# Kernel optimization log

Measured on AMD Instinct MI355X. Metric: run time of the kernel, lower is better.

The kernel has to match this reference:

```python
import jax, jax.numpy as jnp
import numpy as np

B, H, W, C = 4, 64, 64, 512
R = max(1, C // 8)  # reduced = channels // 8

def setup_inputs() -> dict:
    key = jax.random.key(0)
    ks = jax.random.split(key, 5)
    x  = jax.random.normal(ks[0], (B, H, W, C), dtype=jnp.float32)
    Wq = jax.random.normal(ks[1], (C, R), dtype=jnp.float32) * (1.0 / np.sqrt(C))
    Wk = jax.random.normal(ks[2], (C, R), dtype=jnp.float32) * (1.0 / np.sqrt(C))
    Wv = jax.random.normal(ks[3], (C, C), dtype=jnp.float32) * (1.0 / np.sqrt(C))
    Wo = jax.random.normal(ks[4], (C, C), dtype=jnp.float32) * (1.0 / np.sqrt(C))
    gamma = jnp.float32(1.0)
    return {"x": x, "Wq": Wq, "Wk": Wk, "Wv": Wv, "Wo": Wo, "gamma": gamma}

def reference(x, Wq, Wk, Wv, Wo, gamma):
    b, h, w, c = x.shape
    hw = h * w
    r = Wq.shape[1]
    xf = x.reshape(b, hw, c)                      # [B, HW, C]; 1x1 conv == channel matmul
    q = xf @ Wq                                   # [B, HW, R]
    k = xf @ Wk                                   # [B, HW, R]
    v = xf @ Wv                                   # [B, HW, C]
    scale = jnp.sqrt(jnp.asarray(r, dtype=x.dtype))
    scores = jnp.einsum('bnr,bmr->bnm', q, k) / scale   # [B, HW, HW]
    attn = jax.nn.softmax(scores, axis=-1)
    attended = jnp.einsum('bnm,bmc->bnc', attn, v)      # [B, HW, C]
    out = attended @ Wo                                  # out_conv (1x1, no bias)
    return (gamma * out.reshape(b, h, w, c) + x)
```

## Files before the change

kernel.cpp:

```cpp
#include <hip/hip_runtime.h>

typedef unsigned short u16;
typedef short short8 __attribute__((ext_vector_type(8)));
typedef float f32x4 __attribute__((ext_vector_type(4)));

#define LOG2E 1.44269504088896340736f

__device__ __forceinline__ u16 f2bf(float f) {
  unsigned u = __builtin_bit_cast(unsigned, f);
  u += 0x7fffu + ((u >> 16) & 1u);
  return (u16)(u >> 16);
}

__device__ __forceinline__ unsigned cvt_pk_bf16(float lo, float hi) {
  unsigned r;
  asm("v_cvt_pk_bf16_f32 %0, %1, %2" : "=v"(r) : "v"(lo), "v"(hi));
  return r;
}

__global__ __launch_bounds__(256) void k_convert_x(const float* __restrict__ x,
                                                   u16* __restrict__ xb) {
  int i = blockIdx.x * 256 + threadIdx.x;
  float4 v = ((const float4*)x)[i];
  ushort4 o;
  o.x = f2bf(v.x); o.y = f2bf(v.y); o.z = f2bf(v.z); o.w = f2bf(v.w);
  ((ushort4*)xb)[i] = o;
}

__global__ __launch_bounds__(256) void k_wcat(const float* __restrict__ Wq,
                                              const float* __restrict__ Wk,
                                              const float* __restrict__ Wv,
                                              const float* __restrict__ Wo,
                                              u16* __restrict__ wcatT) {
  __shared__ float wo8T[8 * 512];
  int bid = blockIdx.x, t = threadIdx.x;
  if (bid < 8) {
    for (int i = t; i < 8192; i += 256) {
      int j = bid * 16 + (i >> 9);
      int c = i & 511;
      float v = (j < 64) ? Wq[c * 64 + j] * (0.125f * LOG2E) : Wk[c * 64 + (j - 64)];
      wcatT[j * 512 + c] = f2bf(v);
    }
  } else {
    int j0 = (bid - 8) * 8;
    for (int i = t; i < 4096; i += 256) {
      int jj = i >> 9, kk = i & 511;
      wo8T[jj * 512 + kk] = Wo[kk * 512 + j0 + jj];
    }
    __syncthreads();
    for (int c = t; c < 512; c += 256) {
      const float4* wr = (const float4*)(Wv + c * 512);
      float acc[8] = {};
      for (int kk = 0; kk < 128; kk++) {
        float4 v = wr[kk];
#pragma unroll
        for (int jj = 0; jj < 8; jj++) {
          float4 wa = *(const float4*)&wo8T[jj * 512 + kk * 4];
          acc[jj] += v.x * wa.x + v.y * wa.y + v.z * wa.z + v.w * wa.w;
        }
      }
#pragma unroll
      for (int jj = 0; jj < 8; jj++)
        wcatT[(128 + j0 + jj) * 512 + c] = f2bf(acc[jj]);
    }
  }
}

__global__ __launch_bounds__(256) void k_qkv(const u16* __restrict__ xb,
                                             const u16* __restrict__ wcatT,
                                             u16* __restrict__ q,
                                             u16* __restrict__ kf,
                                             u16* __restrict__ vf) {
  __shared__ u16 lds[16384];
  int tid = threadIdx.x;
  int w = tid >> 6, lane = tid & 63;
  int fr = lane & 15, fg = lane >> 4;
  int wm = w >> 1, wn = w & 1;
  int rowbase = blockIdx.y * 128;
  int jbase = blockIdx.x * 128;
  f32x4 acc[4][4] = {};

  for (int kb = 0; kb < 512; kb += 64) {
    __syncthreads();
#pragma unroll
    for (int n = 0; n < 4; n++) {
      int lin = n * 4096 + tid * 16;
      int row = lin >> 7;
      int src = (((lin >> 4) & 7) * 16) ^ ((row & 7) << 4);
      const char* ga = (const char*)(xb + (size_t)(rowbase + row) * 512 + kb) + src;
      __builtin_amdgcn_global_load_lds(
          (const __attribute__((address_space(1))) void*)ga,
          (__attribute__((address_space(3))) void*)((char*)lds + n * 4096 + (w << 10)),
          16, 0, 0);
    }
#pragma unroll
    for (int n = 0; n < 4; n++) {
      int lin = n * 4096 + tid * 16;
      int row = lin >> 7;
      int src = (((lin >> 4) & 7) * 16) ^ ((row & 7) << 4);
      const char* ga = (const char*)(wcatT + (size_t)(jbase + row) * 512 + kb) + src;
      __builtin_amdgcn_global_load_lds(
          (const __attribute__((address_space(1))) void*)ga,
          (__attribute__((address_space(3))) void*)((char*)lds + 16384 + n * 4096 + (w << 10)),
          16, 0, 0);
    }
    __syncthreads();
    short8 af[4][2], bfr[4][2];
#pragma unroll
    for (int mt = 0; mt < 4; mt++)
#pragma unroll
      for (int ks = 0; ks < 2; ks++) {
        int row = wm * 64 + mt * 16 + fr;
        int off = row * 128 + ((ks * 64 + fg * 16) ^ ((row & 7) << 4));
        af[mt][ks] = *(const short8*)((const char*)lds + off);
      }
#pragma unroll
    for (int nt = 0; nt < 4; nt++)
#pragma unroll
      for (int ks = 0; ks < 2; ks++) {
        int j = wn * 64 + nt * 16 + fr;
        int off = 16384 + j * 128 + ((ks * 64 + fg * 16) ^ ((j & 7) << 4));
        bfr[nt][ks] = *(const short8*)((const char*)lds + off);
      }
#pragma unroll
    for (int ks = 0; ks < 2; ks++)
#pragma unroll
      for (int mt = 0; mt < 4; mt++)
#pragma unroll
        for (int nt = 0; nt < 4; nt++)
          acc[mt][nt] = __builtin_amdgcn_mfma_f32_16x16x32_bf16(
              af[mt][ks], bfr[nt][ks], acc[mt][nt], 0, 0, 0);
  }

  if (jbase < 128) {
    int r0 = rowbase + wm * 64, j0 = jbase + wn * 64;
    if (wn == 0) {
#pragma unroll
      for (int mt = 0; mt < 4; mt++)
#pragma unroll
        for (int nt = 0; nt < 4; nt++) {
          int j16 = j0 + nt * 16 + fr;
#pragma unroll
          for (int ii = 0; ii < 4; ii++) {
            int rg = r0 + mt * 16 + fg * 4 + ii;
            q[rg * 64 + j16] = f2bf(acc[mt][nt][ii]);
          }
        }
    } else {
      int bb = r0 >> 12;
      int kt = (r0 & 4095) >> 6;
#pragma unroll
      for (int mt = 0; mt < 4; mt++)
#pragma unroll
        for (int nt = 0; nt < 4; nt++) {
          int dd = nt * 16 + fr;
          int sl = dd >> 5, fgk = (dd & 31) >> 3, e = dd & 7;
#pragma unroll
          for (int ii = 0; ii < 4; ii++) {
            size_t idx = ((((size_t)((bb * 64 + kt) * 4 + mt) * 2 + sl) * 16 +
                           (fg * 4 + ii)) * 32) + fgk * 8 + e;
            kf[idx] = f2bf(acc[mt][nt][ii]);
          }
        }
    }
  } else {
    int bb = rowbase >> 12;
    int ktb = ((rowbase & 4095) >> 6) + wm;
    int cbase = (jbase - 128) + wn * 64;
#pragma unroll
    for (int nt = 0; nt < 4; nt++) {
      int c = cbase + nt * 16 + fr;
      int ct = c >> 4;
#pragma unroll
      for (int mp = 0; mp < 2; mp++) {
        uint4 u;
        u.x = cvt_pk_bf16(acc[2 * mp][nt][0], acc[2 * mp][nt][1]);
        u.y = cvt_pk_bf16(acc[2 * mp][nt][2], acc[2 * mp][nt][3]);
        u.z = cvt_pk_bf16(acc[2 * mp + 1][nt][0], acc[2 * mp + 1][nt][1]);
        u.w = cvt_pk_bf16(acc[2 * mp + 1][nt][2], acc[2 * mp + 1][nt][3]);
        size_t off16 = (((size_t)((bb * 64 + ktb) * 32 + ct) * 2 + mp) * 16 + fr) * 4 + fg;
        *(uint4*)((char*)vf + off16 * 16) = u;
      }
    }
  }
}

__global__ __launch_bounds__(256, 2) void k_attn(const u16* __restrict__ q,
                                                 const u16* __restrict__ kf,
                                                 const u16* __restrict__ vf,
                                                 const float* __restrict__ x,
                                                 const float* __restrict__ gamma_p,
                                                 float* __restrict__ out) {
  int bi = blockIdx.x;
  int xcd = bi & 7, b = xcd >> 1;
  int qt = ((bi >> 3) << 1) | (xcd & 1);
  int qbase = qt * 32;

  int tid = threadIdx.x;
  int w = tid >> 6, lane = tid & 63;
  int fr = lane & 15, fg = lane >> 4;
  int c0 = w * 128;

  short8 qa[2][2];
#pragma unroll
  for (int rt = 0; rt < 2; rt++) {
    const u16* qp = q + ((size_t)((b << 12) + qbase + rt * 16 + fr)) * 64 + fg * 8;
    qa[rt][0] = *(const short8*)qp;
    qa[rt][1] = *(const short8*)(qp + 32);
  }

  f32x4 o[2][8] = {};
  float mR[2] = {-1e30f, -1e30f};
  float lR[2] = {0.f, 0.f};
  const f32x4 zero4 = {};

  const char* kfb = (const char*)(kf + ((size_t)b << 18)) + fr * 64 + fg * 16;
  const char* vfb = (const char*)(vf + ((size_t)b << 21)) + (w * 8) * 2048 + fr * 64 + fg * 16;

#define LOADKC(DST, T)                                                       \
  {                                                                          \
    const char* kp_ = kfb + (size_t)(T) * 8192;                              \
    _Pragma("unroll") for (int kb_ = 0; kb_ < 4; kb_++)                      \
        _Pragma("unroll") for (int sl_ = 0; sl_ < 2; sl_++)                  \
            DST[kb_][sl_] = *(const short8*)(kp_ + kb_ * 2048 + sl_ * 1024); \
  }

#define BODY(T, KU, KP)                                                                   \
  {                                                                                       \
    const char* vp = vfb + (size_t)(T) * 65536;                                           \
    f32x4 s[2][4];                                                                        \
    _Pragma("unroll") for (int rt = 0; rt < 2; rt++)                                      \
        _Pragma("unroll") for (int kb = 0; kb < 4; kb++)                                  \
            s[rt][kb] = __builtin_amdgcn_mfma_f32_16x16x32_bf16(KU[kb][0], qa[rt][0],     \
                                                                zero4, 0, 0, 0);          \
    _Pragma("unroll") for (int rt = 0; rt < 2; rt++)                                      \
        _Pragma("unroll") for (int kb = 0; kb < 4; kb++)                                  \
            s[rt][kb] = __builtin_amdgcn_mfma_f32_16x16x32_bf16(KU[kb][1], qa[rt][1],     \
                                                                s[rt][kb], 0, 0, 0);      \
    LOADKC(KP, ((T) + 1) & 63);                                                           \
    short8 vaA[4][2];                                                                     \
    _Pragma("unroll") for (int nt = 0; nt < 4; nt++)                                      \
        _Pragma("unroll") for (int ks = 0; ks < 2; ks++)                                  \
            vaA[nt][ks] = *(const short8*)(vp + nt * 2048 + ks * 1024);                   \
    short8 pk[2][2];                                                                      \
    _Pragma("unroll") for (int rt = 0; rt < 2; rt++) {                                    \
      float tm = s[rt][0][0];                                                             \
      _Pragma("unroll") for (int kb = 0; kb < 4; kb++)                                    \
          _Pragma("unroll") for (int ii = 0; ii < 4; ii++)                                \
              tm = fmaxf(tm, s[rt][kb][ii]);                                              \
      tm = fmaxf(tm, __shfl_xor(tm, 16));                                                 \
      tm = fmaxf(tm, __shfl_xor(tm, 32));                                                 \
      float m = mR[rt];                                                                   \
      if (__builtin_expect(__any(tm > m + 8.0f), 0)) {                                    \
        float mn = fmaxf(m, tm);                                                          \
        float cr = exp2f(m - mn);                                                         \
        _Pragma("unroll") for (int nt = 0; nt < 8; nt++)                                  \
            _Pragma("unroll") for (int ii = 0; ii < 4; ii++) o[rt][nt][ii] *= cr;         \
        lR[rt] *= cr;                                                                     \
        m = mn;                                                                           \
        mR[rt] = mn;                                                                      \
      }                                                                                   \
      float p[4][4];                                                                      \
      float ts = 0.f;                                                                     \
      _Pragma("unroll") for (int kb = 0; kb < 4; kb++)                                    \
          _Pragma("unroll") for (int ii = 0; ii < 4; ii++) {                              \
        p[kb][ii] = exp2f(s[rt][kb][ii] - m);                                             \
        ts += p[kb][ii];                                                                  \
      }                                                                                   \
      ts += __shfl_xor(ts, 16);                                                           \
      ts += __shfl_xor(ts, 32);                                                           \
      lR[rt] += ts;                                                                       \
      _Pragma("unroll") for (int ks = 0; ks < 2; ks++) {                                  \
        int4 pi;                                                                          \
        pi.x = (int)cvt_pk_bf16(p[2 * ks][0], p[2 * ks][1]);                              \
        pi.y = (int)cvt_pk_bf16(p[2 * ks][2], p[2 * ks][3]);                              \
        pi.z = (int)cvt_pk_bf16(p[2 * ks + 1][0], p[2 * ks + 1][1]);                      \
        pi.w = (int)cvt_pk_bf16(p[2 * ks + 1][2], p[2 * ks + 1][3]);                      \
        pk[rt][ks] = __builtin_bit_cast(short8, pi);                                      \
      }                                                                                   \
    }                                                                                     \
    short8 vaB[4][2];                                                                     \
    _Pragma("unroll") for (int nt = 0; nt < 4; nt++)                                      \
        _Pragma("unroll") for (int ks = 0; ks < 2; ks++)                                  \
            vaB[nt][ks] = *(const short8*)(vp + (nt + 4) * 2048 + ks * 1024);             \
    __builtin_amdgcn_s_setprio(1);                                                        \
    _Pragma("unroll") for (int nt = 0; nt < 4; nt++) {                                    \
      o[0][nt] = __builtin_amdgcn_mfma_f32_16x16x32_bf16(vaA[nt][0], pk[0][0], o[0][nt], 0, 0, 0); \
      o[0][nt] = __builtin_amdgcn_mfma_f32_16x16x32_bf16(vaA[nt][1], pk[0][1], o[0][nt], 0, 0, 0); \
      o[1][nt] = __builtin_amdgcn_mfma_f32_16x16x32_bf16(vaA[nt][0], pk[1][0], o[1][nt], 0, 0, 0); \
      o[1][nt] = __builtin_amdgcn_mfma_f32_16x16x32_bf16(vaA[nt][1], pk[1][1], o[1][nt], 0, 0, 0); \
    }                                                                                     \
    _Pragma("unroll") for (int nt = 0; nt < 4; nt++) {                                    \
      o[0][nt + 4] = __builtin_amdgcn_mfma_f32_16x16x32_bf16(vaB[nt][0], pk[0][0], o[0][nt + 4], 0, 0, 0); \
      o[0][nt + 4] = __builtin_amdgcn_mfma_f32_16x16x32_bf16(vaB[nt][1], pk[0][1], o[0][nt + 4], 0, 0, 0); \
      o[1][nt + 4] = __builtin_amdgcn_mfma_f32_16x16x32_bf16(vaB[nt][0], pk[1][0], o[1][nt + 4], 0, 0, 0); \
      o[1][nt + 4] = __builtin_amdgcn_mfma_f32_16x16x32_bf16(vaB[nt][1], pk[1][1], o[1][nt + 4], 0, 0, 0); \
    }                                                                                     \
    __builtin_amdgcn_s_setprio(0);                                                        \
  }

  short8 kcA[4][2], kcB[4][2];
  LOADKC(kcA, 0);
  for (int kt = 0; kt < 64; kt += 2) {
    BODY(kt, kcA, kcB);
    BODY(kt + 1, kcB, kcA);
  }

  float g = gamma_p[0];
#pragma unroll
  for (int rt = 0; rt < 2; rt++) {
    float il = 1.0f / lR[rt];
    size_t row = (size_t)((b << 12) + qbase + rt * 16 + fr);
#pragma unroll
    for (int nt = 0; nt < 8; nt++) {
      size_t idx = row * 512 + c0 + nt * 16 + fg * 4;
      float4 xo = *(const float4*)(x + idx);
      float4 r;
      r.x = g * o[rt][nt][0] * il + xo.x;
      r.y = g * o[rt][nt][1] * il + xo.y;
      r.z = g * o[rt][nt][2] * il + xo.z;
      r.w = g * o[rt][nt][3] * il + xo.w;
      *(float4*)(out + idx) = r;
    }
  }
#undef BODY
#undef LOADKC
}

extern "C" void kernel_launch(void* const* d_in, const int* in_sizes, int n_in,
                              void* d_out, int out_size, void* d_ws, size_t ws_size,
                              hipStream_t stream) {
  const float* x  = (const float*)d_in[0];
  const float* Wq = (const float*)d_in[1];
  const float* Wk = (const float*)d_in[2];
  const float* Wv = (const float*)d_in[3];
  const float* Wo = (const float*)d_in[4];
  const float* gm = (const float*)d_in[5];
  float* out = (float*)d_out;

  char* ws = (char*)d_ws;
  u16* xb    = (u16*)(ws);
  u16* wcatT = (u16*)(ws + 16777216);
  u16* q     = (u16*)(ws + 17432576);
  u16* kf    = (u16*)(ws + 19529728);
  u16* vf    = (u16*)(ws + 21626880);

  hipLaunchKernelGGL(k_convert_x, dim3(8192), dim3(256), 0, stream, x, xb);
  hipLaunchKernelGGL(k_wcat, dim3(72), dim3(256), 0, stream, Wq, Wk, Wv, Wo, wcatT);
  hipLaunchKernelGGL(k_qkv, dim3(5, 128), dim3(256), 0, stream, xb, wcatT, q, kf, vf);
  hipLaunchKernelGGL(k_attn, dim3(512), dim3(256), 0, stream, q, kf, vf, x, gm, out);
}
```

Baseline: 359.7 us.

## Split attention into single-wave blocks, use fast exp2, defer row-sum reduction, stage q/k stores

The attention kernel now launches one wave per block, with the wave index taken from the block id, instead of four waves per block. The softmax uses the hardware exp2 and rcp intrinsics. Row sums are accumulated per lane and shuffle-reduced once after the loop rather than every tile. In the QKV projection, q and k outputs are staged through LDS and written as coalesced 16-byte stores instead of scattered 2-byte stores. Precision changes slightly from the approximate exp, and the block reshaping alters occupancy and scheduling.

Result: slower. 1.077 ms (+199.3%).

```diff
diff --git a/kernel.cpp b/kernel.cpp
--- a/kernel.cpp
+++ b/kernel.cpp
@@ -16,6 +16,16 @@
   unsigned r;
   asm("v_cvt_pk_bf16_f32 %0, %1, %2" : "=v"(r) : "v"(lo), "v"(hi));
   return r;
+}
+
+__device__ __forceinline__ float fast_exp2(float x) {
+#if __has_builtin(__builtin_amdgcn_exp2f)
+  return __builtin_amdgcn_exp2f(x);
+#else
+  float r;
+  asm("v_exp_f32 %0, %1" : "=v"(r) : "v"(x));
+  return r;
+#endif
 }
 
 __global__ __launch_bounds__(256) void k_convert_x(const float* __restrict__ x,
@@ -71,7 +81,7 @@
                                              u16* __restrict__ q,
                                              u16* __restrict__ kf,
                                              u16* __restrict__ vf) {
-  __shared__ u16 lds[16384];
+  __shared__ alignas(16) u16 lds[16384];
   int tid = threadIdx.x;
   int w = tid >> 6, lane = tid & 63;
   int fr = lane & 15, fg = lane >> 4;
@@ -133,35 +143,37 @@
   }
 
   if (jbase < 128) {
-    int r0 = rowbase + wm * 64, j0 = jbase + wn * 64;
-    if (wn == 0) {
-#pragma unroll
-      for (int mt = 0; mt < 4; mt++)
-#pragma unroll
-        for (int nt = 0; nt < 4; nt++) {
-          int j16 = j0 + nt * 16 + fr;
-#pragma unroll
-          for (int ii = 0; ii < 4; ii++) {
-            int rg = r0 + mt * 16 + fg * 4 + ii;
-            q[rg * 64 + j16] = f2bf(acc[mt][nt][ii]);
-          }
+    __syncthreads();
+    int base = wn ? 8192 : 0;
+#pragma unroll
+    for (int mt = 0; mt < 4; mt++)
+#pragma unroll
+      for (int nt = 0; nt < 4; nt++) {
+        int dd = nt * 16 + fr;
+#pragma unroll
+        for (int ii = 0; ii < 4; ii++) {
+          int rl = wm * 64 + mt * 16 + fg * 4 + ii;
+          lds[base + rl * 64 + dd] = f2bf(acc[mt][nt][ii]);
         }
-    } else {
-      int bb = r0 >> 12;
-      int kt = (r0 & 4095) >> 6;
-#pragma unroll
-      for (int mt = 0; mt < 4; mt++)
-#pragma unroll
-        for (int nt = 0; nt < 4; nt++) {
-          int dd = nt * 16 + fr;
-          int sl = dd >> 5, fgk = (dd & 31) >> 3, e = dd & 7;
-#pragma unroll
-          for (int ii = 0; ii < 4; ii++) {
-            size_t idx = ((((size_t)((bb * 64 + kt) * 4 + mt) * 2 + sl) * 16 +
-                           (fg * 4 + ii)) * 32) + fgk * 8 + e;
-            kf[idx] = f2bf(acc[mt][nt][ii]);
-          }
-        }
+      }
+    __syncthreads();
+    size_t qoff = (size_t)rowbase * 64;
+#pragma unroll
+    for (int c = 0; c < 4; c++) {
+      int ch = c * 256 + tid;
+      *(uint4*)(q + qoff + ch * 8) = *(const uint4*)&lds[ch * 8];
+    }
+    int bb = rowbase >> 12;
+    int kt0 = (rowbase & 4095) >> 6;
+#pragma unroll
+    for (int c = 0; c < 4; c++) {
+      int ch = c * 256 + tid;
+      int ktl = ch >> 9, r = ch & 511;
+      int kb2 = r >> 7, sl = (r >> 6) & 1, frp = (r >> 2) & 15, fgk = r & 3;
+      int key = ktl * 64 + kb2 * 16 + frp;
+      int d = sl * 32 + fgk * 8;
+      uint4 v = *(const uint4*)&lds[8192 + key * 64 + d];
+      *(uint4*)(kf + ((size_t)(bb * 64 + kt0 + ktl)) * 4096 + r * 8) = v;
     }
   } else {
     int bb = rowbase >> 12;
@@ -185,19 +197,20 @@
   }
 }
 
-__global__ __launch_bounds__(256, 2) void k_attn(const u16* __restrict__ q,
-                                                 const u16* __restrict__ kf,
-                                                 const u16* __restrict__ vf,
-                                                 const float* __restrict__ x,
-                                                 const float* __restrict__ gamma_p,
-                                                 float* __restrict__ out) {
+__global__ __launch_bounds__(64, 4) void k_attn(const u16* __restrict__ q,
+                                                const u16* __restrict__ kf,
+                                                const u16* __restrict__ vf,
+                                                const float* __restrict__ x,
+                                                const float* __restrict__ gamma_p,
+                                                float* __restrict__ out) {
   int bi = blockIdx.x;
   int xcd = bi & 7, b = xcd >> 1;
-  int qt = ((bi >> 3) << 1) | (xcd & 1);
+  int idx = bi >> 3;
+  int w = idx & 3;
+  int qt = (((idx >> 2) & 63) << 1) | (xcd & 1);
   int qbase = qt * 32;
 
-  int tid = threadIdx.x;
-  int w = tid >> 6, lane = tid & 63;
+  int lane = threadIdx.x;
   int fr = lane & 15, fg = lane >> 4;
   int c0 = w * 128;
 
@@ -211,7 +224,7 @@
 
   f32x4 o[2][8] = {};
   float mR[2] = {-1e30f, -1e30f};
-  float lR[2] = {0.f, 0.f};
+  float lsum[2] = {0.f, 0.f};
   const f32x4 zero4 = {};
 
   const char* kfb = (const char*)(kf + ((size_t)b << 18)) + fr * 64 + fg * 16;
@@ -244,32 +257,32 @@
             vaA[nt][ks] = *(const short8*)(vp + nt * 2048 + ks * 1024);                   \
     short8 pk[2][2];                                                                      \
     _Pragma("unroll") for (int rt = 0; rt < 2; rt++) {                                    \
-      float tm = s[rt][0][0];                                                             \
-      _Pragma("unroll") for (int kb = 0; kb < 4; kb++)                                    \
-          _Pragma("unroll") for (int ii = 0; ii < 4; ii++)                                \
-              tm = fmaxf(tm, s[rt][kb][ii]);                                              \
+      float t0 = fmaxf(fmaxf(s[rt][0][0], s[rt][0][1]), fmaxf(s[rt][0][2], s[rt][0][3])); \
+      float t1 = fmaxf(fmaxf(s[rt][1][0], s[rt][1][1]), fmaxf(s[rt][1][2], s[rt][1][3])); \
+      float t2 = fmaxf(fmaxf(s[rt][2][0], s[rt][2][1]), fmaxf(s[rt][2][2], s[rt][2][3])); \
+      float t3 = fmaxf(fmaxf(s[rt][3][0], s[rt][3][1]), fmaxf(s[rt][3][2], s[rt][3][3])); \
+      float tm = fmaxf(fmaxf(t0, t1), fmaxf(t2, t3));                                     \
       tm = fmaxf(tm, __shfl_xor(tm, 16));                                                 \
       tm = fmaxf(tm, __shfl_xor(tm, 32));                                                 \
       float m = mR[rt];                                                                   \
       if (__builtin_expect(__any(tm > m + 8.0f), 0)) {                                    \
         float mn = fmaxf(m, tm);                                                          \
-        float cr = exp2f(m - mn);                                                         \
+        float cr = fast_exp2(m - mn);                                                     \
         _Pragma("unroll") for (int nt = 0; nt < 8; nt++)                                  \
             _Pragma("unroll") for (int ii = 0; ii < 4; ii++) o[rt][nt][ii] *= cr;         \
-        lR[rt] *= cr;                                                                     \
+        lsum[rt] *= cr;                                                                   \
         m = mn;                                                                           \
         mR[rt] = mn;                                                                      \
       }                                                                                   \
       float p[4][4];                                                                      \
-      float ts = 0.f;                                                                     \
       _Pragma("unroll") for (int kb = 0; kb < 4; kb++)                                    \
-          _Pragma("unroll") for (int ii = 0; ii < 4; ii++) {                              \
-        p[kb][ii] = exp2f(s[rt][kb][ii] - m);                                             \
-        ts += p[kb][ii];                                                                  \
-      }                                                                                   \
-      ts += __shfl_xor(ts, 16);                                                           \
-      ts += __shfl_xor(ts, 32);                                                           \
-      lR[rt] += ts;                                                                       \
+          _Pragma("unroll") for (int ii = 0; ii < 4; ii++)                                \
+              p[kb][ii] = fast_exp2(s[rt][kb][ii] - m);                                   \
+      float u0 = (p[0][0] + p[0][1]) + (p[0][2] + p[0][3]);                               \
+      float u1 = (p[1][0] + p[1][1]) + (p[1][2] + p[1][3]);                               \
+      float u2 = (p[2][0] + p[2][1]) + (p[2][2] + p[2][3]);                               \
+      float u3 = (p[3][0] + p[3][1]) + (p[3][2] + p[3][3]);                               \
+      lsum[rt] += (u0 + u1) + (u2 + u3);                                                  \
       _Pragma("unroll") for (int ks = 0; ks < 2; ks++) {                                  \
         int4 pi;                                                                          \
         pi.x = (int)cvt_pk_bf16(p[2 * ks][0], p[2 * ks][1]);                              \
@@ -309,18 +322,21 @@
   float g = gamma_p[0];
 #pragma unroll
   for (int rt = 0; rt < 2; rt++) {
-    float il = 1.0f / lR[rt];
+    float ts = lsum[rt];
+    ts += __shfl_xor(ts, 16);
+    ts += __shfl_xor(ts, 32);
+    float il = __builtin_amdgcn_rcpf(ts);
     size_t row = (size_t)((b << 12) + qbase + rt * 16 + fr);
 #pragma unroll
     for (int nt = 0; nt < 8; nt++) {
-      size_t idx = row * 512 + c0 + nt * 16 + fg * 4;
-      float4 xo = *(const float4*)(x + idx);
+      size_t idxg = row * 512 + c0 + nt * 16 + fg * 4;
+      float4 xo = *(const float4*)(x + idxg);
       float4 r;
       r.x = g * o[rt][nt][0] * il + xo.x;
       r.y = g * o[rt][nt][1] * il + xo.y;
       r.z = g * o[rt][nt][2] * il + xo.z;
       r.w = g * o[rt][nt][3] * il + xo.w;
-      *(float4*)(out + idx) = r;
+      *(float4*)(out + idxg) = r;
     }
   }
 #undef BODY
@@ -348,5 +364,5 @@
   hipLaunchKernelGGL(k_convert_x, dim3(8192), dim3(256), 0, stream, x, xb);
   hipLaunchKernelGGL(k_wcat, dim3(72), dim3(256), 0, stream, Wq, Wk, Wv, Wo, wcatT);
   hipLaunchKernelGGL(k_qkv, dim3(5, 128), dim3(256), 0, stream, xb, wcatT, q, kf, vf);
-  hipLaunchKernelGGL(k_attn, dim3(512), dim3(256), 0, stream, q, kf, vf, x, gm, out);
-}
+  hipLaunchKernelGGL(k_attn, dim3(2048), dim3(64), 0, stream, q, kf, vf, x, gm, out);
+}
```
